# Optimization experiments

Measured on AMD Instinct MI355X. Metric: run time of the kernel, lower is better.

Reference implementation:

```python
import jax, jax.numpy as jnp
import numpy as np

EMB = 768
HEADS = 8

def setup_inputs() -> dict:
    key = jax.random.key(0)
    ks = jax.random.split(key, 5)
    x = jax.random.normal(ks[0], (8, 2048, EMB), dtype=jnp.float32)
    s = 1.0 / np.sqrt(EMB)
    W_qkv = jax.random.normal(ks[1], (EMB, 3 * EMB), dtype=jnp.float32) * s
    b_qkv = jnp.zeros((3 * EMB,), dtype=jnp.float32)
    W_proj = jax.random.normal(ks[2], (EMB, EMB), dtype=jnp.float32) * s
    b_proj = jnp.zeros((EMB,), dtype=jnp.float32)
    return {"x": x, "W_qkv": W_qkv, "b_qkv": b_qkv, "W_proj": W_proj, "b_proj": b_proj}

def reference(x, W_qkv, b_qkv, W_proj, b_proj):
    B, N, E = x.shape
    H = HEADS
    D = E // H
    qkv = x @ W_qkv + b_qkv  # [B, N, 3E]
    q, k, v = jnp.split(qkv, 3, axis=-1)
    # [B, N, E] -> [B, H, N, D]
    def heads(t):
        return t.reshape(B, N, H, D).transpose(0, 2, 1, 3)
    q, k, v = heads(q), heads(k), heads(v)
    # NOTE: original scales by 1/sqrt(emb_size), not 1/sqrt(head_dim)
    dots = jnp.einsum('bhnd,bhmd->bhnm', q, k) / jnp.sqrt(jnp.float32(E))
    attn = jax.nn.softmax(dots, axis=-1)  # dropout inactive (eval mode)
    out = jnp.einsum('bhnm,bhmd->bhnd', attn, v)
    out = out.transpose(0, 2, 1, 3).reshape(B, N, E)
    return out @ W_proj + b_proj
```

## Files before the change

### kernel.cpp

```cpp
#include <hip/hip_runtime.h>
#include <hip/hip_bf16.h>

typedef __attribute__((ext_vector_type(8))) short bf16x8;
typedef __attribute__((ext_vector_type(4))) short bf16x4;
typedef __attribute__((ext_vector_type(4))) float f32x4;
typedef __attribute__((ext_vector_type(16))) float f32x16;
typedef __attribute__((ext_vector_type(4))) unsigned int uint4v;

__device__ __forceinline__ short f2bf(float f) {
    unsigned int u = __float_as_uint(f);
    u += 0x7FFFu + ((u >> 16) & 1u);
    return (short)(u >> 16);
}

__device__ __forceinline__ unsigned cvtpk(float lo, float hi) {
    unsigned r;
    asm("v_cvt_pk_bf16_f32 %0, %1, %2" : "=v"(r) : "v"(lo), "v"(hi));
    return r;
}

__global__ __launch_bounds__(256) void cast_kernel(const float* __restrict__ in,
                                                   short* __restrict__ out, int n4) {
    int i = blockIdx.x * 256 + threadIdx.x;
    if (i >= n4) return;
    const f32x4 v = *(const f32x4*)(in + (size_t)i * 4);
    bf16x4 o;
    o[0] = f2bf(v[0]); o[1] = f2bf(v[1]); o[2] = f2bf(v[2]); o[3] = f2bf(v[3]);
    *(bf16x4*)(out + (size_t)i * 4) = o;
}

__global__ __launch_bounds__(256) void transpose_cast_kernel(const float* __restrict__ W,
                                                             short* __restrict__ WT,
                                                             int R, int C) {
    __shared__ float tile[64][65];
    const int bc = blockIdx.x * 64;
    const int br = blockIdx.y * 64;
    const int t = threadIdx.x;
#pragma unroll
    for (int i = 0; i < 16; ++i) {
        int o = t + 256 * i;
        int r = o >> 6, c = o & 63;
        tile[r][c] = W[(size_t)(br + r) * C + bc + c];
    }
    __syncthreads();
#pragma unroll
    for (int i = 0; i < 16; ++i) {
        int o = t + 256 * i;
        int c = o >> 6, r = o & 63;
        WT[(size_t)(bc + c) * R + br + r] = f2bf(tile[r][c]);
    }
}

#define GPAD 72
__global__ __launch_bounds__(256, 2) void gemm1_kernel(
    const short* __restrict__ A, const short* __restrict__ BT,
    const float* __restrict__ bias,
    short* __restrict__ Qh, short* __restrict__ Kh, short* __restrict__ Vt)
{
    __shared__ short As[128][GPAD];
    __shared__ short Bs[128][GPAD];
    const int K = 768;
    const int t = threadIdx.x;
    const int w = t >> 6, l = t & 63;
    const int wr = w >> 1, wc = w & 1;
    const int lr = l & 15, lg = l >> 4;

    const size_t Abase = (size_t)blockIdx.x * 128 * K;
    const size_t Bbase = (size_t)blockIdx.y * 128 * K;

    const f32x4 z4 = {0.f, 0.f, 0.f, 0.f};
    f32x4 acc[4][4];
#pragma unroll
    for (int i = 0; i < 4; ++i)
#pragma unroll
        for (int j = 0; j < 4; ++j) acc[i][j] = z4;

    for (int kt = 0; kt < K; kt += 64) {
#pragma unroll
        for (int i = 0; i < 4; ++i) {
            int o = t + 256 * i;
            int r = o >> 3, kc = o & 7;
            *(bf16x8*)&As[r][kc * 8] = *(const bf16x8*)(A + Abase + (size_t)r * K + kt + kc * 8);
            *(bf16x8*)&Bs[r][kc * 8] = *(const bf16x8*)(BT + Bbase + (size_t)r * K + kt + kc * 8);
        }
        __syncthreads();
#pragma unroll
        for (int kk = 0; kk < 2; ++kk) {
            bf16x8 af[4], bfr[4];
#pragma unroll
            for (int mi = 0; mi < 4; ++mi)
                af[mi] = *(const bf16x8*)&As[wr * 64 + mi * 16 + lr][kk * 32 + lg * 8];
#pragma unroll
            for (int ni = 0; ni < 4; ++ni)
                bfr[ni] = *(const bf16x8*)&Bs[wc * 64 + ni * 16 + lr][kk * 32 + lg * 8];
#pragma unroll
            for (int mi = 0; mi < 4; ++mi)
#pragma unroll
                for (int ni = 0; ni < 4; ++ni)
                    acc[mi][ni] = __builtin_amdgcn_mfma_f32_16x16x32_bf16(
                        af[mi], bfr[ni], acc[mi][ni], 0, 0, 0);
        }
        __syncthreads();
    }

    const float qs = 0.05205877f;
    const int rb = blockIdx.x * 128 + wr * 64;
    const int cb = blockIdx.y * 128 + wc * 64;
#pragma unroll
    for (int ni = 0; ni < 4; ++ni) {
        const int c = cb + ni * 16 + lr;
        const float bv = bias[c];
        const int which = (c >= 1536) ? 2 : (c >= 768 ? 1 : 0);
        const int cc = c - which * 768;
        const int h = cc / 96;
        const int d = cc - h * 96;
#pragma unroll
        for (int mi = 0; mi < 4; ++mi) {
            const int r0 = rb + mi * 16 + lg * 4;
            const int b = r0 >> 11, n0 = r0 & 2047;
            const int hb = b * 8 + h;
            if (which == 2) {
                bf16x4 pk;
#pragma unroll
                for (int r = 0; r < 4; ++r) pk[r] = f2bf(acc[mi][ni][r] + bv);
                *(bf16x4*)&Vt[((size_t)hb * 96 + d) * 2048 + n0] = pk;
            } else if (which == 1) {
#pragma unroll
                for (int r = 0; r < 4; ++r)
                    Kh[((size_t)hb * 2048 + n0 + r) * 96 + d] = f2bf(acc[mi][ni][r] + bv);
            } else {
#pragma unroll
                for (int r = 0; r < 4; ++r)
                    Qh[((size_t)hb * 2048 + n0 + r) * 96 + d] = f2bf((acc[mi][ni][r] + bv) * qs);
            }
        }
    }
}

__global__ __launch_bounds__(256, 2) void attn_kernel(
    const short* __restrict__ Qh, const short* __restrict__ Kh,
    const short* __restrict__ Vt, short* __restrict__ AO)
{
    __shared__ __align__(16) char smem[54272];
    short (*Ks0)[104] = (short (*)[104])smem;
    short (*Ks1)[104] = (short (*)[104])(smem + 13312);
    short (*Vs0)[72]  = (short (*)[72])(smem + 26624);
    short (*Vs1)[72]  = (short (*)[72])(smem + 40448);
    short (*Qs)[104]  = (short (*)[104])smem;
    __shared__ float ltab[4][32];

    const int t = threadIdx.x;
    const int w = t >> 6, l = t & 63;
    const int ql = l & 31, hi = l >> 5;

    const unsigned L = blockIdx.y * 16 + blockIdx.x;
    const int bh = (int)((L & 7) + 8 * (L >> 7));
    const int qt = (int)((L >> 3) & 15);

    const short* Qg = Qh + (size_t)bh * 2048 * 96 + (size_t)qt * 128 * 96;
    const short* Kg = Kh + (size_t)bh * 2048 * 96;
    const short* Vg = Vt + (size_t)bh * 96 * 2048;

    bf16x8 kreg[3], vreg[3];
#pragma unroll
    for (int i = 0; i < 3; ++i) {
        int o = t + 256 * i;
        kreg[i] = *(const bf16x8*)(Kg + 8 * (size_t)o);
        vreg[i] = *(const bf16x8*)(Vg + (size_t)(o >> 3) * 2048 + (o & 7) * 8);
    }

#pragma unroll
    for (int i = 0; i < 6; ++i) {
        int o = t + 256 * i;
        *(bf16x8*)&Qs[o / 12][(o % 12) * 8] = *(const bf16x8*)(Qg + 8 * (size_t)o);
    }
    __syncthreads();
    bf16x8 qf[6];
#pragma unroll
    for (int kk = 0; kk < 6; ++kk)
        qf[kk] = *(const bf16x8*)&Qs[w * 32 + ql][kk * 16 + hi * 8];
    __syncthreads();

#pragma unroll
    for (int i = 0; i < 3; ++i) {
        int o = t + 256 * i;
        *(bf16x8*)&Ks0[o / 12][(o % 12) * 8] = kreg[i];
        *(bf16x8*)&Vs0[o >> 3][(o & 7) * 8] = vreg[i];
    }
#pragma unroll
    for (int i = 0; i < 3; ++i) {
        int o = t + 256 * i;
        kreg[i] = *(const bf16x8*)(Kg + (size_t)64 * 96 + 8 * (size_t)o);
        vreg[i] = *(const bf16x8*)(Vg + (size_t)(o >> 3) * 2048 + 64 + (o & 7) * 8);
    }
    __syncthreads();

    f32x16 oacc[3];
#pragma unroll
    for (int i = 0; i < 3; ++i)
#pragma unroll
        for (int r = 0; r < 16; ++r) oacc[i][r] = 0.f;
    float lacc = 0.f;

    auto iter = [&](int kt, short (*rK)[104], short (*rV)[72],
                    short (*wK)[104], short (*wV)[72]) {
        if (kt < 31) {
#pragma unroll
            for (int i = 0; i < 3; ++i) {
                int o = t + 256 * i;
                *(bf16x8*)&wK[o / 12][(o % 12) * 8] = kreg[i];
                *(bf16x8*)&wV[o >> 3][(o & 7) * 8] = vreg[i];
            }
        }
        if (kt < 30) {
            const size_t koff = (size_t)(kt + 2) * 64 * 96;
            const int moff = (kt + 2) * 64;
#pragma unroll
            for (int i = 0; i < 3; ++i) {
                int o = t + 256 * i;
                kreg[i] = *(const bf16x8*)(Kg + koff + 8 * (size_t)o);
                vreg[i] = *(const bf16x8*)(Vg + (size_t)(o >> 3) * 2048 + moff + (o & 7) * 8);
            }
        }

        f32x16 sa0, sa1;
#pragma unroll
        for (int r = 0; r < 16; ++r) { sa0[r] = 0.f; sa1[r] = 0.f; }
        __builtin_amdgcn_s_setprio(1);
#pragma unroll
        for (int kk = 0; kk < 6; ++kk) {
            bf16x8 kf0 = *(const bf16x8*)&rK[ql][kk * 16 + hi * 8];
            bf16x8 kf1 = *(const bf16x8*)&rK[32 + ql][kk * 16 + hi * 8];
            sa0 = __builtin_amdgcn_mfma_f32_32x32x16_bf16(kf0, qf[kk], sa0, 0, 0, 0);
            sa1 = __builtin_amdgcn_mfma_f32_32x32x16_bf16(kf1, qf[kk], sa1, 0, 0, 0);
        }
        __builtin_amdgcn_s_setprio(0);

        bf16x8 pa[4];
#pragma unroll
        for (int mi = 0; mi < 2; ++mi) {
            float p[16];
#pragma unroll
            for (int r = 0; r < 16; ++r) {
                p[r] = __builtin_amdgcn_exp2f(mi == 0 ? sa0[r] : sa1[r]);
                lacc += p[r];
            }
            unsigned x0 = cvtpk(p[0], p[1]),  y0 = cvtpk(p[4], p[5]);
            unsigned x1 = cvtpk(p[2], p[3]),  y1 = cvtpk(p[6], p[7]);
            unsigned x2 = cvtpk(p[8], p[9]),  y2 = cvtpk(p[12], p[13]);
            unsigned x3 = cvtpk(p[10], p[11]), y3 = cvtpk(p[14], p[15]);
            asm("v_permlane32_swap_b32 %0, %1" : "+v"(x0), "+v"(y0));
            asm("v_permlane32_swap_b32 %0, %1" : "+v"(x1), "+v"(y1));
            asm("v_permlane32_swap_b32 %0, %1" : "+v"(x2), "+v"(y2));
            asm("v_permlane32_swap_b32 %0, %1" : "+v"(x3), "+v"(y3));
            uint4v uA; uA[0] = x0; uA[1] = x1; uA[2] = y0; uA[3] = y1;
            uint4v uB; uB[0] = x2; uB[1] = x3; uB[2] = y2; uB[3] = y3;
            pa[mi * 2 + 0] = __builtin_bit_cast(bf16x8, uA);
            pa[mi * 2 + 1] = __builtin_bit_cast(bf16x8, uB);
        }

        __builtin_amdgcn_s_setprio(1);
#pragma unroll
        for (int kb = 0; kb < 4; ++kb) {
#pragma unroll
            for (int db = 0; db < 3; ++db) {
                bf16x8 vf = *(const bf16x8*)&rV[db * 32 + ql][kb * 16 + hi * 8];
                oacc[db] = __builtin_amdgcn_mfma_f32_32x32x16_bf16(pa[kb], vf, oacc[db], 0, 0, 0);
            }
        }
        __builtin_amdgcn_s_setprio(0);
        __syncthreads();
    };

    for (int kt = 0; kt < 32; kt += 2) {
        iter(kt,     Ks0, Vs0, Ks1, Vs1);
        iter(kt + 1, Ks1, Vs1, Ks0, Vs0);
    }

    float lsum = lacc + __shfl_xor(lacc, 32);
    if (l < 32) ltab[w][l] = lsum;
    asm volatile("s_waitcnt lgkmcnt(0)" ::: "memory");

    float linv[16];
#pragma unroll
    for (int r = 0; r < 16; ++r) {
        const int q = (r & 3) + 8 * (r >> 2) + 4 * hi;
        linv[r] = 1.0f / ltab[w][q];
    }

    const int b = bh >> 3, h = bh & 7;
    const size_t rowbase = (size_t)b * 2048 + qt * 128 + w * 32;
#pragma unroll
    for (int db = 0; db < 3; ++db) {
#pragma unroll
        for (int r = 0; r < 16; ++r) {
            const int q = (r & 3) + 8 * (r >> 2) + 4 * hi;
            AO[(rowbase + q) * 768 + h * 96 + db * 32 + ql] = f2bf(oacc[db][r] * linv[r]);
        }
    }
}

__global__ __launch_bounds__(256, 2) void gemm2_kernel(
    const short* __restrict__ A, const short* __restrict__ BT,
    const float* __restrict__ bias, float* __restrict__ out)
{
    __shared__ short As[128][GPAD];
    __shared__ short Bs[128][GPAD];
    const int K = 768;
    const int t = threadIdx.x;
    const int w = t >> 6, l = t & 63;
    const int wr = w >> 1, wc = w & 1;
    const int lr = l & 15, lg = l >> 4;

    const size_t Abase = (size_t)blockIdx.x * 128 * K;
    const size_t Bbase = (size_t)blockIdx.y * 128 * K;

    const f32x4 z4 = {0.f, 0.f, 0.f, 0.f};
    f32x4 acc[4][4];
#pragma unroll
    for (int i = 0; i < 4; ++i)
#pragma unroll
        for (int j = 0; j < 4; ++j) acc[i][j] = z4;

    for (int kt = 0; kt < K; kt += 64) {
#pragma unroll
        for (int i = 0; i < 4; ++i) {
            int o = t + 256 * i;
            int r = o >> 3, kc = o & 7;
            *(bf16x8*)&As[r][kc * 8] = *(const bf16x8*)(A + Abase + (size_t)r * K + kt + kc * 8);
            *(bf16x8*)&Bs[r][kc * 8] = *(const bf16x8*)(BT + Bbase + (size_t)r * K + kt + kc * 8);
        }
        __syncthreads();
#pragma unroll
        for (int kk = 0; kk < 2; ++kk) {
            bf16x8 af[4], bfr[4];
#pragma unroll
            for (int mi = 0; mi < 4; ++mi)
                af[mi] = *(const bf16x8*)&As[wr * 64 + mi * 16 + lr][kk * 32 + lg * 8];
#pragma unroll
            for (int ni = 0; ni < 4; ++ni)
                bfr[ni] = *(const bf16x8*)&Bs[wc * 64 + ni * 16 + lr][kk * 32 + lg * 8];
#pragma unroll
            for (int mi = 0; mi < 4; ++mi)
#pragma unroll
                for (int ni = 0; ni < 4; ++ni)
                    acc[mi][ni] = __builtin_amdgcn_mfma_f32_16x16x32_bf16(
                        af[mi], bfr[ni], acc[mi][ni], 0, 0, 0);
        }
        __syncthreads();
    }

    const int rb = blockIdx.x * 128 + wr * 64;
    const int cb = blockIdx.y * 128 + wc * 64;
#pragma unroll
    for (int ni = 0; ni < 4; ++ni) {
        const int c = cb + ni * 16 + lr;
        const float bv = bias[c];
#pragma unroll
        for (int mi = 0; mi < 4; ++mi) {
            const int r0 = rb + mi * 16 + lg * 4;
#pragma unroll
            for (int r = 0; r < 4; ++r)
                out[(size_t)(r0 + r) * 768 + c] = acc[mi][ni][r] + bv;
        }
    }
}

extern "C" void kernel_launch(void* const* d_in, const int* in_sizes, int n_in,
                              void* d_out, int out_size, void* d_ws, size_t ws_size,
                              hipStream_t stream) {
    const float* x     = (const float*)d_in[0];
    const float* Wqkv  = (const float*)d_in[1];
    const float* bqkv  = (const float*)d_in[2];
    const float* Wproj = (const float*)d_in[3];
    const float* bproj = (const float*)d_in[4];
    float* out = (float*)d_out;

    char* ws = (char*)d_ws;
    short* xb     = (short*)(ws);
    short* WqkvT  = (short*)(ws + 25165824);
    short* WprojT = (short*)(ws + 28704768);
    short* Qh     = (short*)(ws + 29884416);
    short* Kh     = (short*)(ws + 55050240);
    short* Vt     = (short*)(ws + 80216064);
    short* AO     = xb;

    cast_kernel<<<12288, 256, 0, stream>>>(x, xb, 3145728);
    transpose_cast_kernel<<<dim3(36, 12), 256, 0, stream>>>(Wqkv, WqkvT, 768, 2304);
    transpose_cast_kernel<<<dim3(12, 12), 256, 0, stream>>>(Wproj, WprojT, 768, 768);
    gemm1_kernel<<<dim3(128, 18), 256, 0, stream>>>(xb, WqkvT, bqkv, Qh, Kh, Vt);
    attn_kernel<<<dim3(16, 64), 256, 0, stream>>>(Qh, Kh, Vt, AO);
    gemm2_kernel<<<dim3(128, 6), 256, 0, stream>>>(AO, WprojT, bproj, out);
}
```

Baseline: 237.5 us.

## Process 64 query rows per wave in attention to reuse K/V fragments

Each attention block now covers 256 queries instead of 128, so each wave owns two 32-row query groups. Every K and V fragment read from LDS feeds MFMAs for both groups, which halves shared-memory traffic per MFMA. The grid is halved and the softmax row-sum bookkeeping and output normalization are extended to cover both groups. In exchange, register pressure roughly doubles for the accumulators and Q fragments, which risks lower occupancy or spills, and there are fewer blocks to spread across the CUs.

```diff
diff --git a/kernel.cpp b/kernel.cpp
--- a/kernel.cpp
+++ b/kernel.cpp
@@ -147,17 +147,17 @@
     short (*Vs0)[72]  = (short (*)[72])(smem + 26624);
     short (*Vs1)[72]  = (short (*)[72])(smem + 40448);
     short (*Qs)[104]  = (short (*)[104])smem;
-    __shared__ float ltab[4][32];
+    __shared__ float ltab[4][64];
 
     const int t = threadIdx.x;
     const int w = t >> 6, l = t & 63;
     const int ql = l & 31, hi = l >> 5;
 
-    const unsigned L = blockIdx.y * 16 + blockIdx.x;
-    const int bh = (int)((L & 7) + 8 * (L >> 7));
-    const int qt = (int)((L >> 3) & 15);
-
-    const short* Qg = Qh + (size_t)bh * 2048 * 96 + (size_t)qt * 128 * 96;
+    const unsigned L = blockIdx.y * 8 + blockIdx.x;
+    const int bh = (int)((L & 7) + 8 * (L >> 6));
+    const int qt = (int)((L >> 3) & 7);
+
+    const short* Qg = Qh + (size_t)bh * 2048 * 96 + (size_t)qt * 256 * 96;
     const short* Kg = Kh + (size_t)bh * 2048 * 96;
     const short* Vg = Vt + (size_t)bh * 96 * 2048;
 
@@ -170,15 +170,17 @@
     }
 
 #pragma unroll
-    for (int i = 0; i < 6; ++i) {
+    for (int i = 0; i < 12; ++i) {
         int o = t + 256 * i;
         *(bf16x8*)&Qs[o / 12][(o % 12) * 8] = *(const bf16x8*)(Qg + 8 * (size_t)o);
     }
     __syncthreads();
-    bf16x8 qf[6];
-#pragma unroll
-    for (int kk = 0; kk < 6; ++kk)
-        qf[kk] = *(const bf16x8*)&Qs[w * 32 + ql][kk * 16 + hi * 8];
+    bf16x8 qfA[6], qfB[6];
+#pragma unroll
+    for (int kk = 0; kk < 6; ++kk) {
+        qfA[kk] = *(const bf16x8*)&Qs[w * 64 + ql][kk * 16 + hi * 8];
+        qfB[kk] = *(const bf16x8*)&Qs[w * 64 + 32 + ql][kk * 16 + hi * 8];
+    }
     __syncthreads();
 
 #pragma unroll
@@ -195,12 +197,12 @@
     }
     __syncthreads();
 
-    f32x16 oacc[3];
+    f32x16 oaccA[3], oaccB[3];
 #pragma unroll
     for (int i = 0; i < 3; ++i)
 #pragma unroll
-        for (int r = 0; r < 16; ++r) oacc[i][r] = 0.f;
-    float lacc = 0.f;
+        for (int r = 0; r < 16; ++r) { oaccA[i][r] = 0.f; oaccB[i][r] = 0.f; }
+    float laccA = 0.f, laccB = 0.f;
 
     auto iter = [&](int kt, short (*rK)[104], short (*rV)[72],
                     short (*wK)[104], short (*wV)[72]) {
@@ -223,52 +225,56 @@
             }
         }
 
-        f32x16 sa0, sa1;
-#pragma unroll
-        for (int r = 0; r < 16; ++r) { sa0[r] = 0.f; sa1[r] = 0.f; }
-        __builtin_amdgcn_s_setprio(1);
-#pragma unroll
-        for (int kk = 0; kk < 6; ++kk) {
-            bf16x8 kf0 = *(const bf16x8*)&rK[ql][kk * 16 + hi * 8];
-            bf16x8 kf1 = *(const bf16x8*)&rK[32 + ql][kk * 16 + hi * 8];
-            sa0 = __builtin_amdgcn_mfma_f32_32x32x16_bf16(kf0, qf[kk], sa0, 0, 0, 0);
-            sa1 = __builtin_amdgcn_mfma_f32_32x32x16_bf16(kf1, qf[kk], sa1, 0, 0, 0);
-        }
-        __builtin_amdgcn_s_setprio(0);
-
-        bf16x8 pa[4];
-#pragma unroll
-        for (int mi = 0; mi < 2; ++mi) {
-            float p[16];
-#pragma unroll
-            for (int r = 0; r < 16; ++r) {
-                p[r] = __builtin_amdgcn_exp2f(mi == 0 ? sa0[r] : sa1[r]);
-                lacc += p[r];
-            }
-            unsigned x0 = cvtpk(p[0], p[1]),  y0 = cvtpk(p[4], p[5]);
-            unsigned x1 = cvtpk(p[2], p[3]),  y1 = cvtpk(p[6], p[7]);
-            unsigned x2 = cvtpk(p[8], p[9]),  y2 = cvtpk(p[12], p[13]);
-            unsigned x3 = cvtpk(p[10], p[11]), y3 = cvtpk(p[14], p[15]);
-            asm("v_permlane32_swap_b32 %0, %1" : "+v"(x0), "+v"(y0));
-            asm("v_permlane32_swap_b32 %0, %1" : "+v"(x1), "+v"(y1));
-            asm("v_permlane32_swap_b32 %0, %1" : "+v"(x2), "+v"(y2));
-            asm("v_permlane32_swap_b32 %0, %1" : "+v"(x3), "+v"(y3));
-            uint4v uA; uA[0] = x0; uA[1] = x1; uA[2] = y0; uA[3] = y1;
-            uint4v uB; uB[0] = x2; uB[1] = x3; uB[2] = y2; uB[3] = y3;
-            pa[mi * 2 + 0] = __builtin_bit_cast(bf16x8, uA);
-            pa[mi * 2 + 1] = __builtin_bit_cast(bf16x8, uB);
-        }
-
-        __builtin_amdgcn_s_setprio(1);
-#pragma unroll
-        for (int kb = 0; kb < 4; ++kb) {
-#pragma unroll
-            for (int db = 0; db < 3; ++db) {
-                bf16x8 vf = *(const bf16x8*)&rV[db * 32 + ql][kb * 16 + hi * 8];
-                oacc[db] = __builtin_amdgcn_mfma_f32_32x32x16_bf16(pa[kb], vf, oacc[db], 0, 0, 0);
-            }
-        }
-        __builtin_amdgcn_s_setprio(0);
+#pragma unroll
+        for (int kvh = 0; kvh < 2; ++kvh) {
+            f32x16 saA, saB;
+#pragma unroll
+            for (int r = 0; r < 16; ++r) { saA[r] = 0.f; saB[r] = 0.f; }
+            __builtin_amdgcn_s_setprio(1);
+#pragma unroll
+            for (int kk = 0; kk < 6; ++kk) {
+                bf16x8 kf = *(const bf16x8*)&rK[kvh * 32 + ql][kk * 16 + hi * 8];
+                saA = __builtin_amdgcn_mfma_f32_32x32x16_bf16(kf, qfA[kk], saA, 0, 0, 0);
+                saB = __builtin_amdgcn_mfma_f32_32x32x16_bf16(kf, qfB[kk], saB, 0, 0, 0);
+            }
+            __builtin_amdgcn_s_setprio(0);
+
+            bf16x8 pa[2][2];
+#pragma unroll
+            for (int g = 0; g < 2; ++g) {
+                float p[16];
+#pragma unroll
+                for (int r = 0; r < 16; ++r)
+                    p[r] = __builtin_amdgcn_exp2f(g == 0 ? saA[r] : saB[r]);
+                float s = ((p[0] + p[1]) + (p[2] + p[3])) + ((p[4] + p[5]) + (p[6] + p[7]))
+                        + ((p[8] + p[9]) + (p[10] + p[11])) + ((p[12] + p[13]) + (p[14] + p[15]));
+                if (g == 0) laccA += s; else laccB += s;
+                unsigned x0 = cvtpk(p[0], p[1]),   y0 = cvtpk(p[4], p[5]);
+                unsigned x1 = cvtpk(p[2], p[3]),   y1 = cvtpk(p[6], p[7]);
+                unsigned x2 = cvtpk(p[8], p[9]),   y2 = cvtpk(p[12], p[13]);
+                unsigned x3 = cvtpk(p[10], p[11]), y3 = cvtpk(p[14], p[15]);
+                asm("v_permlane32_swap_b32 %0, %1" : "+v"(x0), "+v"(y0));
+                asm("v_permlane32_swap_b32 %0, %1" : "+v"(x1), "+v"(y1));
+                asm("v_permlane32_swap_b32 %0, %1" : "+v"(x2), "+v"(y2));
+                asm("v_permlane32_swap_b32 %0, %1" : "+v"(x3), "+v"(y3));
+                uint4v uA; uA[0] = x0; uA[1] = x1; uA[2] = y0; uA[3] = y1;
+                uint4v uB; uB[0] = x2; uB[1] = x3; uB[2] = y2; uB[3] = y3;
+                pa[g][0] = __builtin_bit_cast(bf16x8, uA);
+                pa[g][1] = __builtin_bit_cast(bf16x8, uB);
+            }
+
+            __builtin_amdgcn_s_setprio(1);
+#pragma unroll
+            for (int kb = 0; kb < 2; ++kb) {
+#pragma unroll
+                for (int db = 0; db < 3; ++db) {
+                    bf16x8 vf = *(const bf16x8*)&rV[db * 32 + ql][(kvh * 2 + kb) * 16 + hi * 8];
+                    oaccA[db] = __builtin_amdgcn_mfma_f32_32x32x16_bf16(pa[0][kb], vf, oaccA[db], 0, 0, 0);
+                    oaccB[db] = __builtin_amdgcn_mfma_f32_32x32x16_bf16(pa[1][kb], vf, oaccB[db], 0, 0, 0);
+                }
+            }
+            __builtin_amdgcn_s_setprio(0);
+        }
         __syncthreads();
     };
 
@@ -277,25 +283,25 @@
         iter(kt + 1, Ks1, Vs1, Ks0, Vs0);
     }
 
-    float lsum = lacc + __shfl_xor(lacc, 32);
-    if (l < 32) ltab[w][l] = lsum;
+    float lsumA = laccA + __shfl_xor(laccA, 32);
+    float lsumB = laccB + __shfl_xor(laccB, 32);
+    if (hi == 0) ltab[w][ql] = lsumA;
+    else         ltab[w][32 + ql] = lsumB;
     asm volatile("s_waitcnt lgkmcnt(0)" ::: "memory");
 
-    float linv[16];
-#pragma unroll
-    for (int r = 0; r < 16; ++r) {
-        const int q = (r & 3) + 8 * (r >> 2) + 4 * hi;
-        linv[r] = 1.0f / ltab[w][q];
-    }
-
     const int b = bh >> 3, h = bh & 7;
-    const size_t rowbase = (size_t)b * 2048 + qt * 128 + w * 32;
-#pragma unroll
-    for (int db = 0; db < 3; ++db) {
-#pragma unroll
-        for (int r = 0; r < 16; ++r) {
-            const int q = (r & 3) + 8 * (r >> 2) + 4 * hi;
-            AO[(rowbase + q) * 768 + h * 96 + db * 32 + ql] = f2bf(oacc[db][r] * linv[r]);
+    const size_t rowbase = (size_t)b * 2048 + qt * 256 + w * 64;
+#pragma unroll
+    for (int g = 0; g < 2; ++g) {
+        const f32x16* oacc = g ? oaccB : oaccA;
+#pragma unroll
+        for (int db = 0; db < 3; ++db) {
+#pragma unroll
+            for (int r = 0; r < 16; ++r) {
+                const int q = g * 32 + (r & 3) + 8 * (r >> 2) + 4 * hi;
+                const float li = 1.0f / ltab[w][q];
+                AO[(rowbase + q) * 768 + h * 96 + db * 32 + ql] = f2bf(oacc[db][r] * li);
+            }
         }
     }
 }
@@ -389,6 +395,6 @@
     transpose_cast_kernel<<<dim3(36, 12), 256, 0, stream>>>(Wqkv, WqkvT, 768, 2304);
     transpose_cast_kernel<<<dim3(12, 12), 256, 0, stream>>>(Wproj, WprojT, 768, 768);
     gemm1_kernel<<<dim3(128, 18), 256, 0, stream>>>(xb, WqkvT, bqkv, Qh, Kh, Vt);
-    attn_kernel<<<dim3(16, 64), 256, 0, stream>>>(Qh, Kh, Vt, AO);
+    attn_kernel<<<dim3(8, 64), 256, 0, stream>>>(Qh, Kh, Vt, AO);
     gemm2_kernel<<<dim3(128, 6), 256, 0, stream>>>(AO, WprojT, bproj, out);
 }
```

Result: slower. 263.1 us (+10.8%).
